# Kernel optimization log

Hardware: AMD Instinct MI355X
Metric: run time of the kernel (lower is better)

## Reference

```python
import jax, jax.numpy as jnp
import numpy as np
import math

NQ = 8            # n_qubits (hardcoded in _TransformerBlockQuantum)
DIM = 2 ** NQ     # statevector size = 256
H = 16            # num_heads
EPS = 1e-5        # LayerNorm eps

# PauliZ expectation table: wire 0 = most significant bit. ZTAB[w, j] = +/-1
_bits = (np.arange(DIM)[None, :] >> (NQ - 1 - np.arange(NQ)[:, None])) & 1
ZTAB = (1.0 - 2.0 * _bits).astype(np.float32)  # [NQ, DIM]


def _apply_1q(state, gate, w):
    # state: [N, 2^NQ] complex, gate: [N, 2, 2] complex, acts on wire w (MSB ordering)
    N = state.shape[0]
    s = state.reshape(N, 2 ** w, 2, 2 ** (NQ - w - 1))
    s = jnp.einsum('nab,npbq->npaq', gate, s)
    return s.reshape(N, DIM)


def _apply_cnot(state, c):
    # CNOT with control wire c, target wire c+1 (adjacent chain)
    N = state.shape[0]
    s = state.reshape(N, 2 ** c, 2, 2, 2 ** (NQ - c - 2))
    s = jnp.concatenate([s[:, :, :1], jnp.flip(s[:, :, 1:], axis=3)], axis=2)
    return s.reshape(N, DIM)


def _layernorm(x, g, b):
    mu = jnp.mean(x, axis=-1, keepdims=True)
    var = jnp.mean((x - mu) ** 2, axis=-1, keepdims=True)
    return (x - mu) / jnp.sqrt(var + EPS) * g + b


def _quantum_ffn(x, Win, b_in, Wout, b_out, ry):
    B, S, D = x.shape
    ang = (jnp.einsum('bsd,qd->bsq', x, Win) + b_in).reshape(-1, NQ)  # [N, NQ]
    N = ang.shape[0]
    state = jnp.zeros((N, DIM), jnp.complex64).at[:, 0].set(1.0)
    # RX encoding (per-token angles)
    for w in range(NQ):
        th = ang[:, w] * 0.5
        c, s = jnp.cos(th), jnp.sin(th)
        g = jnp.stack([jnp.stack([c, -1j * s], -1), jnp.stack([-1j * s, c], -1)], -2)
        state = _apply_1q(state, g.astype(jnp.complex64), w)
    # trainable RY (shared angles)
    for w in range(NQ):
        th = ry[w] * 0.5
        c, s = jnp.cos(th), jnp.sin(th)
        g = jnp.stack([jnp.stack([c, -s]), jnp.stack([s, c])]).astype(jnp.complex64)
        state = _apply_1q(state, jnp.broadcast_to(g, (N, 2, 2)), w)
    # CNOT entangling chain
    for w in range(NQ - 1):
        state = _apply_cnot(state, w)
    probs = jnp.abs(state) ** 2                      # [N, DIM] float32
    expz = probs @ ZTAB.T                            # [N, NQ]
    out = jnp.einsum('bsq,dq->bsd', expz.reshape(B, S, NQ), Wout) + b_out
    return jax.nn.relu(out)  # dropout = identity in eval


def _forward(x, Wq, Wk, Wv, Wo, g1, b1, g2, b2, Win, b_in, Wout, b_out, ry):
    B, S, D = x.shape
    dk = D // H
    q = jnp.einsum('bsd,ed->bse', x, Wq).reshape(B, S, H, dk)
    k = jnp.einsum('bsd,ed->bse', x, Wk).reshape(B, S, H, dk)
    v = jnp.einsum('bsd,ed->bse', x, Wv).reshape(B, S, H, dk)
    scores = jnp.einsum('bqhd,bkhd->bhqk', q, k) / math.sqrt(dk)
    attn = jax.nn.softmax(scores, axis=-1)
    o = jnp.einsum('bhqk,bkhd->bqhd', attn, v).reshape(B, S, D)
    attn_out = jnp.einsum('bsd,ed->bse', o, Wo)
    x1 = _layernorm(x + attn_out, g1, b1)
    ffn_out = _quantum_ffn(x1, Win, b_in, Wout, b_out, ry)
    return _layernorm(x1 + ffn_out, g2, b2)


def setup_inputs() -> dict:
    key = jax.random.key(0)
    ks = jax.random.split(key, 16)
    B, S, D = 2, 2048, 1024
    sd = 1.0 / math.sqrt(D)
    return {
        'x': jax.random.normal(ks[0], (B, S, D), jnp.float32),
        'Wq': jax.random.normal(ks[1], (D, D), jnp.float32) * sd,
        'Wk': jax.random.normal(ks[2], (D, D), jnp.float32) * sd,
        'Wv': jax.random.normal(ks[3], (D, D), jnp.float32) * sd,
        'Wo': jax.random.normal(ks[4], (D, D), jnp.float32) * sd,
        'g1': jnp.ones((D,), jnp.float32),
        'b1': jnp.zeros((D,), jnp.float32),
        'g2': jnp.ones((D,), jnp.float32),
        'b2': jnp.zeros((D,), jnp.float32),
        'Win': jax.random.normal(ks[5], (NQ, D), jnp.float32) * sd,
        'b_in': jnp.zeros((NQ,), jnp.float32),
        'Wout': jax.random.normal(ks[6], (D, NQ), jnp.float32) * (1.0 / math.sqrt(NQ)),
        'b_out': jnp.zeros((D,), jnp.float32),
        'ry': jax.random.normal(ks[7], (NQ,), jnp.float32) * 0.1,
    }


def reference(x, Wq, Wk, Wv, Wo, g1, b1, g2, b2, Win, b_in, Wout, b_out, ry):
    return _forward(x, Wq, Wk, Wv, Wo, g1, b1, g2, b2, Win, b_in, Wout, b_out, ry)
```

## Files before the change

kernel.cpp:

```cpp
#include <hip/hip_runtime.h>
#include <stdint.h>


typedef unsigned short u16;
typedef unsigned int   u32;
typedef __bf16 bf16x8 __attribute__((ext_vector_type(8)));
typedef u16    u16x8  __attribute__((ext_vector_type(8)));
typedef u16    u16x4  __attribute__((ext_vector_type(4)));
typedef float  f32x4  __attribute__((ext_vector_type(4)));

#define DEV static __device__ __forceinline__

DEV u16 f2b(float f){ u32 u = __float_as_uint(f); return (u16)((u + 0x7fffu + ((u>>16)&1u)) >> 16); }

#define MFMA16(a,b,c) __builtin_amdgcn_mfma_f32_16x16x32_bf16((a),(b),(c),0,0,0)
#define GLD16(gp,lp) __builtin_amdgcn_global_load_lds( \
    (const __attribute__((address_space(1))) u32*)(const void*)(gp), \
    (__attribute__((address_space(3))) u32*)(void*)(lp), 16, 0, 0)

__global__ __launch_bounds__(256) void k_cast(const float* __restrict__ src, u16* __restrict__ dst){
  const int i = blockIdx.x*256 + threadIdx.x;
  const f32x4* s = (const f32x4*)src + (size_t)i*2;
  f32x4 a = s[0], b = s[1];
  u16x8 o;
  o[0]=f2b(a.x); o[1]=f2b(a.y); o[2]=f2b(a.z); o[3]=f2b(a.w);
  o[4]=f2b(b.x); o[5]=f2b(b.y); o[6]=f2b(b.z); o[7]=f2b(b.w);
  ((u16x8*)dst)[i] = o;
}

__global__ __launch_bounds__(256) void k_cast_w(
    const float* __restrict__ Wq, const float* __restrict__ Wk,
    const float* __restrict__ Wv, const float* __restrict__ Wo,
    u16* __restrict__ wb, u16* __restrict__ wob){
  const int r = blockIdx.x >> 9, bi = blockIdx.x & 511;
  const float* src = (r==0)?Wq:((r==1)?Wk:((r==2)?Wv:Wo));
  u16* dst = (r<3) ? (wb + (size_t)r*1048576) : wob;
  const int i = bi*256 + threadIdx.x;
  const f32x4* s = (const f32x4*)src + (size_t)i*2;
  f32x4 a = s[0], b = s[1];
  u16x8 o;
  o[0]=f2b(a.x); o[1]=f2b(a.y); o[2]=f2b(a.z); o[3]=f2b(a.w);
  o[4]=f2b(b.x); o[5]=f2b(b.y); o[6]=f2b(b.z); o[7]=f2b(b.w);
  ((u16x8*)dst)[i] = o;
}

template<int MODE>
__global__ __launch_bounds__(256) void k_gemm_nt(
    const u16* __restrict__ A, const u16* __restrict__ B,
    float* __restrict__ Cf, u16* __restrict__ Qo, u16* __restrict__ Ko, u16* __restrict__ Vt,
    int K, int N)
{
  __shared__ __attribute__((aligned(16))) u16 As[128*64];
  __shared__ __attribute__((aligned(16))) u16 Bs[128*64];
  const int tid = threadIdx.x, lane = tid & 63, w = tid >> 6;
  const int wr = w >> 1, wc = w & 1;
  const int m0 = blockIdx.y*128, n0 = blockIdx.x*128;
  const int l15 = lane & 15, lg = lane >> 4;
  f32x4 acc[4][4] = {};
  const int lr = lane >> 3, lc = (lane & 7)*8;
  const u16* ag = A + (size_t)(m0 + w*32 + lr)*K + lc;
  const u16* bg = B + (size_t)(n0 + w*32 + lr)*K + lc;
  u16* asl = &As[(w*32)*64];
  u16* bsl = &Bs[(w*32)*64];
  for (int k0 = 0; k0 < K; k0 += 64){
    __syncthreads();
    #pragma unroll
    for (int c = 0; c < 4; ++c){
      GLD16(ag + (size_t)(c*8)*K + k0, asl + c*512);
      GLD16(bg + (size_t)(c*8)*K + k0, bsl + c*512);
    }
    __syncthreads();
    #pragma unroll
    for (int kk = 0; kk < 2; ++kk){
      const int ko = kk*32 + lg*8;
      bf16x8 af[4], bf[4];
      #pragma unroll
      for (int t=0;t<4;++t) af[t] = *(const bf16x8*)&As[(wr*64 + t*16 + l15)*64 + ko];
      #pragma unroll
      for (int t=0;t<4;++t) bf[t] = *(const bf16x8*)&Bs[(wc*64 + t*16 + l15)*64 + ko];
      #pragma unroll
      for (int i=0;i<4;++i)
        #pragma unroll
        for (int j=0;j<4;++j)
          acc[i][j] = MFMA16(af[i], bf[j], acc[i][j]);
    }
  }
  const int col0 = n0 + wc*64 + l15;
  const int row0 = m0 + wr*64 + lg*4;
  if (MODE==0){
    const int which = n0 >> 10;
    if (which == 2){
      #pragma unroll
      for (int i=0;i<4;++i){
        const int rr0 = row0 + i*16;
        const int bsel = rr0 >> 11, ss = rr0 & 2047;
        #pragma unroll
        for (int j=0;j<4;++j){
          const int d_loc = (col0 + j*16) & 1023;
          const int hh = d_loc >> 6, dd = d_loc & 63;
          u16x4 pk;
          #pragma unroll
          for (int r=0;r<4;++r) pk[r] = f2b(acc[i][j][r]);
          *(u16x4*)(Vt + ((size_t)((bsel*16 + hh)*64 + dd))*2048 + ss) = pk;
        }
      }
    } else {
      u16* dst = which ? Ko : Qo;
      const float scl = which ? 1.f : 0.125f;
      #pragma unroll
      for (int i=0;i<4;++i)
      #pragma unroll
      for (int j=0;j<4;++j){
        const int cc = (col0 + j*16) & 1023;
        #pragma unroll
        for (int r=0;r<4;++r)
          dst[(size_t)(row0 + i*16 + r)*1024 + cc] = f2b(acc[i][j][r]*scl);
      }
    }
  } else {
    #pragma unroll
    for (int i=0;i<4;++i)
    #pragma unroll
    for (int j=0;j<4;++j){
      const int cc = col0 + j*16;
      #pragma unroll
      for (int r=0;r<4;++r)
        Cf[(size_t)(row0 + i*16 + r)*N + cc] = acc[i][j][r];
    }
  }
}

__global__ __launch_bounds__(256) void k_attn(
    const u16* __restrict__ q, const u16* __restrict__ k,
    const u16* __restrict__ vt, u16* __restrict__ o)
{
  __shared__ __attribute__((aligned(16))) char KVb[2][16384];
  __shared__ __attribute__((aligned(16))) u16 Ps[4][1024];
  const int tid = threadIdx.x, lane = tid & 63, w = tid >> 6;
  const int p = blockIdx.x >> 5, qt = blockIdx.x & 31;
  const int b = p >> 4, h = p & 15;
  const int t0 = b*2048 + qt*64 + w*16;
  const int l15 = lane & 15, lg = lane >> 4;
  const int swz = (l15 & 7) << 4;
  bf16x8 qa[2];
  #pragma unroll
  for (int kk=0;kk<2;++kk)
    qa[kk] = *(const bf16x8*)(q + (size_t)(t0 + l15)*1024 + h*64 + kk*32 + lg*8);
  const char* kgl[2]; const char* vgl[2]; int ldsK[2], ldsV[2];
  #pragma unroll
  for (int i=0;i<2;++i){
    const int s = w*2048 + i*1024 + lane*16;
    const int row = s >> 7;
    const int cb = (s & 127) ^ ((row & 7) << 4);
    kgl[i] = (const char*)k  + ((size_t)(b*2048 + row))*2048 + h*128 + cb;
    vgl[i] = (const char*)vt + ((size_t)(p*64    + row))*4096 + cb;
    ldsK[i] = w*2048 + i*1024;
    ldsV[i] = 8192 + w*2048 + i*1024;
  }
  f32x4 oacc[4] = {};
  float mrow = -1e30f, lrow = 0.f;
  int cur = 0;
  #pragma unroll
  for (int i=0;i<2;++i){ GLD16(kgl[i], KVb[0] + ldsK[i]); GLD16(vgl[i], KVb[0] + ldsV[i]); }
  for (int it = 0; it < 32; ++it){
    __syncthreads();
    if (it < 31){
      const size_t nkv = (size_t)(it+1)*64;
      #pragma unroll
      for (int i=0;i<2;++i){
        GLD16(kgl[i] + nkv*2048, KVb[cur^1] + ldsK[i]);
        GLD16(vgl[i] + nkv*2,    KVb[cur^1] + ldsV[i]);
      }
    }
    const char* Kb = KVb[cur];
    const char* Vb = KVb[cur] + 8192;
    f32x4 sacc[4] = {};
    #pragma unroll
    for (int kk=0;kk<2;++kk){
      const int co = (kk*64 + lg*16) ^ swz;
      bf16x8 kbf[4];
      #pragma unroll
      for (int nt=0;nt<4;++nt) kbf[nt] = *(const bf16x8*)(Kb + (nt*16 + l15)*128 + co);
      #pragma unroll
      for (int nt=0;nt<4;++nt) sacc[nt] = MFMA16(kbf[nt], qa[kk], sacc[nt]);
    }
    float mx = sacc[0][0];
    #pragma unroll
    for (int nt=0;nt<4;++nt)
      #pragma unroll
      for (int r=0;r<4;++r) mx = fmaxf(mx, sacc[nt][r]);
    mx = fmaxf(mx, __shfl_xor(mx, 16));
    mx = fmaxf(mx, __shfl_xor(mx, 32));
    const float mnew = fmaxf(mrow, mx);
    const float scl = __expf(mrow - mnew);
    mrow = mnew;
    float rsum = 0.f;
    #pragma unroll
    for (int nt=0;nt<4;++nt)
      #pragma unroll
      for (int r=0;r<4;++r){ float e = __expf(sacc[nt][r] - mnew); sacc[nt][r] = e; rsum += e; }
    rsum += __shfl_xor(rsum, 16);
    rsum += __shfl_xor(rsum, 32);
    lrow = lrow*scl + rsum;
    char* Pw = (char*)&Ps[w][0];
    #pragma unroll
    for (int nt=0;nt<4;++nt){
      u16x4 pk;
      #pragma unroll
      for (int r=0;r<4;++r) pk[r] = f2b(sacc[nt][r]);
      *(u16x4*)(Pw + l15*128 + (((nt*16 + lg*4)*2) ^ swz)) = pk;
    }
    float sclo[4];
    #pragma unroll
    for (int r=0;r<4;++r) sclo[r] = __shfl(scl, lg*4 + r);
    #pragma unroll
    for (int nt=0;nt<4;++nt)
      #pragma unroll
      for (int r=0;r<4;++r) oacc[nt][r] *= sclo[r];
    #pragma unroll
    for (int kk=0;kk<2;++kk){
      const int co = (kk*64 + lg*16) ^ swz;
      bf16x8 pf = *(const bf16x8*)(Pw + l15*128 + co);
      bf16x8 vf[4];
      #pragma unroll
      for (int nt=0;nt<4;++nt) vf[nt] = *(const bf16x8*)(Vb + (nt*16 + l15)*128 + co);
      #pragma unroll
      for (int nt=0;nt<4;++nt) oacc[nt] = MFMA16(pf, vf[nt], oacc[nt]);
    }
    cur ^= 1;
  }
  float rl[4];
  #pragma unroll
  for (int r=0;r<4;++r){ float lf = __shfl(lrow, lg*4 + r); rl[r] = 1.f/lf; }
  #pragma unroll
  for (int nt=0;nt<4;++nt)
  #pragma unroll
  for (int r=0;r<4;++r)
    o[(size_t)(t0 + lg*4 + r)*1024 + h*64 + nt*16 + l15] = f2b(oacc[nt][r]*rl[r]);
}

__global__ __launch_bounds__(256) void k_tail(
    const float* __restrict__ x, const float* __restrict__ attn,
    const float* __restrict__ g1, const float* __restrict__ b1,
    const float* __restrict__ Win, const float* __restrict__ b_in,
    const float* __restrict__ Wout, const float* __restrict__ b_out,
    const float* __restrict__ ry,
    const float* __restrict__ g2, const float* __restrict__ b2,
    float* __restrict__ out)
{
  const int tid = threadIdx.x, lane = tid & 63, w = tid >> 6;
  const int t = blockIdx.x*4 + w;
  const size_t base = (size_t)t*1024;
  f32x4 yv[4];
  float s1 = 0.f, s2 = 0.f;
  #pragma unroll
  for (int c=0;c<4;++c){
    const int idx = c*256 + lane*4;
    f32x4 xv = *(const f32x4*)(x + base + idx);
    f32x4 av = *(const f32x4*)(attn + base + idx);
    f32x4 y = xv + av;
    yv[c] = y;
    s1 += y.x + y.y + y.z + y.w;
    s2 += y.x*y.x + y.y*y.y + y.z*y.z + y.w*y.w;
  }
  #pragma unroll
  for (int off=32; off; off>>=1){ s1 += __shfl_xor(s1, off); s2 += __shfl_xor(s2, off); }
  {
    const float mu = s1*(1.f/1024.f);
    const float rinv = rsqrtf(s2*(1.f/1024.f) - mu*mu + 1e-5f);
    #pragma unroll
    for (int c=0;c<4;++c){
      const int idx = c*256 + lane*4;
      f32x4 gv = *(const f32x4*)(g1 + idx);
      f32x4 bv = *(const f32x4*)(b1 + idx);
      f32x4 y = yv[c];
      y.x = (y.x-mu)*rinv*gv.x + bv.x;
      y.y = (y.y-mu)*rinv*gv.y + bv.y;
      y.z = (y.z-mu)*rinv*gv.z + bv.z;
      y.w = (y.w-mu)*rinv*gv.w + bv.w;
      yv[c] = y;
    }
  }
  float ang[8];
  #pragma unroll
  for (int qq=0; qq<8; ++qq){
    float acc = 0.f;
    #pragma unroll
    for (int c=0;c<4;++c){
      f32x4 wv = *(const f32x4*)(Win + qq*1024 + c*256 + lane*4);
      acc += wv.x*yv[c].x + wv.y*yv[c].y + wv.z*yv[c].z + wv.w*yv[c].w;
    }
    ang[qq] = acc;
  }
  #pragma unroll
  for (int off=32; off; off>>=1)
    #pragma unroll
    for (int qq=0; qq<8; ++qq) ang[qq] += __shfl_xor(ang[qq], off);
  #pragma unroll
  for (int qq=0; qq<8; ++qq) ang[qq] += b_in[qq];
  float vr[4], vi[4];
  #pragma unroll
  for (int r=0;r<4;++r){ vr[r]=0.f; vi[r]=0.f; }
  if (lane==0) vr[0] = 1.f;
  #pragma unroll
  for (int wi=0; wi<8; ++wi){
    float s, c; __sincosf(ang[wi]*0.5f, &s, &c);
    const int pbit = 7 - wi;
    if (pbit >= 6){
      const int rp = 1 << (pbit-6);
      #pragma unroll
      for (int r=0;r<4;++r) if (!(r & rp)){
        const int r2 = r | rp;
        float ar=vr[r], ai=vi[r], br=vr[r2], bi=vi[r2];
        vr[r]  = c*ar + s*bi;  vi[r]  = c*ai - s*br;
        vr[r2] = c*br + s*ai;  vi[r2] = c*bi - s*ar;
      }
    } else {
      const int msk = 1 << pbit;
      #pragma unroll
      for (int r=0;r<4;++r){
        float orr = __shfl_xor(vr[r], msk);
        float oii = __shfl_xor(vi[r], msk);
        float nr = c*vr[r] + s*oii;
        float ni = c*vi[r] - s*orr;
        vr[r]=nr; vi[r]=ni;
      }
    }
  }
  #pragma unroll
  for (int wi=0; wi<8; ++wi){
    float s, c; __sincosf(ry[wi]*0.5f, &s, &c);
    const int pbit = 7 - wi;
    if (pbit >= 6){
      const int rp = 1 << (pbit-6);
      #pragma unroll
      for (int r=0;r<4;++r) if (!(r & rp)){
        const int r2 = r | rp;
        float ar=vr[r], ai=vi[r], br=vr[r2], bi=vi[r2];
        vr[r]  = c*ar - s*br;  vi[r]  = c*ai - s*bi;
        vr[r2] = s*ar + c*br;  vi[r2] = s*ai + c*bi;
      }
    } else {
      const int msk = 1 << pbit;
      const float sg = (lane & msk) ? s : -s;
      #pragma unroll
      for (int r=0;r<4;++r){
        float orr = __shfl_xor(vr[r], msk);
        float oii = __shfl_xor(vi[r], msk);
        float nr = c*vr[r] + sg*orr;
        float ni = c*vi[r] + sg*oii;
        vr[r]=nr; vi[r]=ni;
      }
    }
  }
  { float tr=vr[2]; vr[2]=vr[3]; vr[3]=tr; float ti=vi[2]; vi[2]=vi[3]; vi[3]=ti; }
  vr[1]=__shfl_xor(vr[1],32); vi[1]=__shfl_xor(vi[1],32);
  vr[3]=__shfl_xor(vr[3],32); vi[3]=__shfl_xor(vi[3],32);
  #pragma unroll
  for (int cn=2; cn<7; ++cn){
    const int pc = 7-cn, pt = pc-1;
    const bool ctl = (lane >> pc) & 1;
    #pragma unroll
    for (int r=0;r<4;++r){
      float tr = __shfl_xor(vr[r], 1<<pt);
      float ti = __shfl_xor(vi[r], 1<<pt);
      if (ctl){ vr[r]=tr; vi[r]=ti; }
    }
  }
  float pr[4];
  #pragma unroll
  for (int r=0;r<4;++r) pr[r] = vr[r]*vr[r] + vi[r]*vi[r];
  float e[8];
  e[0] = (pr[0]+pr[1]) - (pr[2]+pr[3]);
  e[1] = (pr[0]+pr[2]) - (pr[1]+pr[3]);
  const float tot = pr[0]+pr[1]+pr[2]+pr[3];
  #pragma unroll
  for (int wi=2; wi<8; ++wi){
    const int pbit = 7-wi;
    e[wi] = ((lane >> pbit) & 1) ? -tot : tot;
  }
  #pragma unroll
  for (int off=1; off<64; off<<=1)
    #pragma unroll
    for (int i=0;i<8;++i) e[i] += __shfl_xor(e[i], off);
  float yy[4][4];
  s1 = 0.f; s2 = 0.f;
  #pragma unroll
  for (int c=0;c<4;++c){
    const float x1a[4] = {yv[c].x, yv[c].y, yv[c].z, yv[c].w};
    #pragma unroll
    for (int j=0;j<4;++j){
      const int d = c*256 + lane*4 + j;
      f32x4 w0 = *(const f32x4*)(Wout + (size_t)d*8);
      f32x4 w1 = *(const f32x4*)(Wout + (size_t)d*8 + 4);
      float acc = b_out[d];
      acc += w0.x*e[0] + w0.y*e[1] + w0.z*e[2] + w0.w*e[3];
      acc += w1.x*e[4] + w1.y*e[5] + w1.z*e[6] + w1.w*e[7];
      const float y = x1a[j] + fmaxf(acc, 0.f);
      yy[c][j] = y;
      s1 += y; s2 += y*y;
    }
  }
  #pragma unroll
  for (int off=32; off; off>>=1){ s1 += __shfl_xor(s1, off); s2 += __shfl_xor(s2, off); }
  const float mu = s1*(1.f/1024.f);
  const float rinv = rsqrtf(s2*(1.f/1024.f) - mu*mu + 1e-5f);
  #pragma unroll
  for (int c=0;c<4;++c){
    const int idx = c*256 + lane*4;
    f32x4 gv = *(const f32x4*)(g2 + idx);
    f32x4 bv = *(const f32x4*)(b2 + idx);
    f32x4 ov;
    ov.x = (yy[c][0]-mu)*rinv*gv.x + bv.x;
    ov.y = (yy[c][1]-mu)*rinv*gv.y + bv.y;
    ov.z = (yy[c][2]-mu)*rinv*gv.z + bv.z;
    ov.w = (yy[c][3]-mu)*rinv*gv.w + bv.w;
    *(f32x4*)(out + base + idx) = ov;
  }
}

extern "C" void kernel_launch(void* const* d_in, const int* in_sizes, int n_in,
                              void* d_out, int out_size, void* d_ws, size_t ws_size,
                              hipStream_t stream)
{
  const float* x    = (const float*)d_in[0];
  const float* Wq   = (const float*)d_in[1];
  const float* Wk   = (const float*)d_in[2];
  const float* Wv   = (const float*)d_in[3];
  const float* Wo   = (const float*)d_in[4];
  const float* g1   = (const float*)d_in[5];
  const float* b1   = (const float*)d_in[6];
  const float* g2   = (const float*)d_in[7];
  const float* b2   = (const float*)d_in[8];
  const float* Win  = (const float*)d_in[9];
  const float* b_in = (const float*)d_in[10];
  const float* Wout = (const float*)d_in[11];
  const float* b_out= (const float*)d_in[12];
  const float* ry   = (const float*)d_in[13];
  float* out = (float*)d_out;
  char* ws = (char*)d_ws;
  const size_t MB = 1024u*1024u;
  u16* xb  = (u16*)(ws + 0*MB);
  u16* wb  = (u16*)(ws + 8*MB);
  u16* wob = (u16*)(ws + 14*MB);
  u16* qb  = (u16*)(ws + 16*MB);
  u16* kb  = (u16*)(ws + 24*MB);
  u16* vtb = (u16*)(ws + 32*MB);
  u16* ob  = (u16*)(ws + 40*MB);
  float* attn_out = (float*)(ws + 48*MB);

  k_cast<<<2048, 256, 0, stream>>>(x, xb);
  k_cast_w<<<2048, 256, 0, stream>>>(Wq, Wk, Wv, Wo, wb, wob);
  k_gemm_nt<0><<<dim3(24,32), 256, 0, stream>>>(xb, wb, nullptr, qb, kb, vtb, 1024, 3072);
  k_attn<<<1024, 256, 0, stream>>>(qb, kb, vtb, ob);
  k_gemm_nt<1><<<dim3(8,32), 256, 0, stream>>>(ob, wob, attn_out, nullptr, nullptr, nullptr, 1024, 1024);
  k_tail<<<1024, 256, 0, stream>>>(x, attn_out, g1, b1, Win, b_in, Wout, b_out, ry, g2, b2, out);
}
```

Before: 279.2 us.

## Double attention query rows per wave, use exp2 softmax with lazy rescale

Result: faster. 270.4 us (-3.1%).

```diff
diff --git a/kernel.cpp b/kernel.cpp
--- a/kernel.cpp
+++ b/kernel.cpp
@@ -12,6 +12,8 @@
 #define DEV static __device__ __forceinline__
 
 DEV u16 f2b(float f){ u32 u = __float_as_uint(f); return (u16)((u + 0x7fffu + ((u>>16)&1u)) >> 16); }
+DEV u16 b2u(__bf16 h){ union{__bf16 b; u16 u;} c; c.b = h; return c.u; }
+DEV float exp2fast(float x){ return __builtin_amdgcn_exp2f(x); }
 
 #define MFMA16(a,b,c) __builtin_amdgcn_mfma_f32_16x16x32_bf16((a),(b),(c),0,0,0)
 #define GLD16(gp,lp) __builtin_amdgcn_global_load_lds( \
@@ -106,7 +108,7 @@
       }
     } else {
       u16* dst = which ? Ko : Qo;
-      const float scl = which ? 1.f : 0.125f;
+      const float scl = which ? 1.f : 0.125f*1.44269504f;
       #pragma unroll
       for (int i=0;i<4;++i)
       #pragma unroll
@@ -135,17 +137,19 @@
     const u16* __restrict__ vt, u16* __restrict__ o)
 {
   __shared__ __attribute__((aligned(16))) char KVb[2][16384];
-  __shared__ __attribute__((aligned(16))) u16 Ps[4][1024];
+  __shared__ __attribute__((aligned(16))) u16 Ps[4][2048];
   const int tid = threadIdx.x, lane = tid & 63, w = tid >> 6;
-  const int p = blockIdx.x >> 5, qt = blockIdx.x & 31;
+  const int p = blockIdx.x >> 4, qt = blockIdx.x & 15;
   const int b = p >> 4, h = p & 15;
-  const int t0 = b*2048 + qt*64 + w*16;
+  const int t0 = b*2048 + qt*128 + w*32;
   const int l15 = lane & 15, lg = lane >> 4;
   const int swz = (l15 & 7) << 4;
-  bf16x8 qa[2];
+  bf16x8 qa[2][2];
+  #pragma unroll
+  for (int mt=0;mt<2;++mt)
   #pragma unroll
   for (int kk=0;kk<2;++kk)
-    qa[kk] = *(const bf16x8*)(q + (size_t)(t0 + l15)*1024 + h*64 + kk*32 + lg*8);
+    qa[mt][kk] = *(const bf16x8*)(q + (size_t)(t0 + mt*16 + l15)*1024 + h*64 + kk*32 + lg*8);
   const char* kgl[2]; const char* vgl[2]; int ldsK[2], ldsV[2];
   #pragma unroll
   for (int i=0;i<2;++i){
@@ -157,8 +161,8 @@
     ldsK[i] = w*2048 + i*1024;
     ldsV[i] = 8192 + w*2048 + i*1024;
   }
-  f32x4 oacc[4] = {};
-  float mrow = -1e30f, lrow = 0.f;
+  f32x4 oacc[2][4] = {};
+  float mrow[2] = {-1e30f, -1e30f}, lrow[2] = {0.f, 0.f};
   int cur = 0;
   #pragma unroll
   for (int i=0;i<2;++i){ GLD16(kgl[i], KVb[0] + ldsK[i]); GLD16(vgl[i], KVb[0] + ldsV[i]); }
@@ -174,7 +178,7 @@
     }
     const char* Kb = KVb[cur];
     const char* Vb = KVb[cur] + 8192;
-    f32x4 sacc[4] = {};
+    f32x4 sacc[2][4] = {};
     #pragma unroll
     for (int kk=0;kk<2;++kk){
       const int co = (kk*64 + lg*16) ^ swz;
@@ -182,61 +186,90 @@
       #pragma unroll
       for (int nt=0;nt<4;++nt) kbf[nt] = *(const bf16x8*)(Kb + (nt*16 + l15)*128 + co);
       #pragma unroll
-      for (int nt=0;nt<4;++nt) sacc[nt] = MFMA16(kbf[nt], qa[kk], sacc[nt]);
-    }
-    float mx = sacc[0][0];
-    #pragma unroll
-    for (int nt=0;nt<4;++nt)
-      #pragma unroll
-      for (int r=0;r<4;++r) mx = fmaxf(mx, sacc[nt][r]);
-    mx = fmaxf(mx, __shfl_xor(mx, 16));
-    mx = fmaxf(mx, __shfl_xor(mx, 32));
-    const float mnew = fmaxf(mrow, mx);
-    const float scl = __expf(mrow - mnew);
-    mrow = mnew;
-    float rsum = 0.f;
-    #pragma unroll
-    for (int nt=0;nt<4;++nt)
-      #pragma unroll
-      for (int r=0;r<4;++r){ float e = __expf(sacc[nt][r] - mnew); sacc[nt][r] = e; rsum += e; }
-    rsum += __shfl_xor(rsum, 16);
-    rsum += __shfl_xor(rsum, 32);
-    lrow = lrow*scl + rsum;
+      for (int mt=0;mt<2;++mt)
+      #pragma unroll
+      for (int nt=0;nt<4;++nt)
+        sacc[mt][nt] = MFMA16(kbf[nt], qa[mt][kk], sacc[mt][nt]);
+    }
+    float mx[2];
+    #pragma unroll
+    for (int mt=0;mt<2;++mt){
+      float m = sacc[mt][0][0];
+      #pragma unroll
+      for (int nt=0;nt<4;++nt)
+        #pragma unroll
+        for (int r=0;r<4;++r) m = fmaxf(m, sacc[mt][nt][r]);
+      m = fmaxf(m, __shfl_xor(m, 16));
+      m = fmaxf(m, __shfl_xor(m, 32));
+      mx[mt] = m;
+    }
+    const int ok = (mx[0] <= mrow[0] + 8.f) && (mx[1] <= mrow[1] + 8.f);
+    if (!__all(ok)){
+      #pragma unroll
+      for (int mt=0;mt<2;++mt){
+        const float mnew = fmaxf(mrow[mt], mx[mt]);
+        const float scl = exp2fast(mrow[mt] - mnew);
+        mrow[mt] = mnew;
+        lrow[mt] *= scl;
+        float sclo[4];
+        #pragma unroll
+        for (int r=0;r<4;++r) sclo[r] = __shfl(scl, lg*4 + r);
+        #pragma unroll
+        for (int nt=0;nt<4;++nt)
+          #pragma unroll
+          for (int r=0;r<4;++r) oacc[mt][nt][r] *= sclo[r];
+      }
+    }
     char* Pw = (char*)&Ps[w][0];
     #pragma unroll
-    for (int nt=0;nt<4;++nt){
-      u16x4 pk;
-      #pragma unroll
-      for (int r=0;r<4;++r) pk[r] = f2b(sacc[nt][r]);
-      *(u16x4*)(Pw + l15*128 + (((nt*16 + lg*4)*2) ^ swz)) = pk;
-    }
-    float sclo[4];
-    #pragma unroll
-    for (int r=0;r<4;++r) sclo[r] = __shfl(scl, lg*4 + r);
-    #pragma unroll
-    for (int nt=0;nt<4;++nt)
-      #pragma unroll
-      for (int r=0;r<4;++r) oacc[nt][r] *= sclo[r];
+    for (int mt=0;mt<2;++mt){
+      float rsum = 0.f;
+      #pragma unroll
+      for (int nt=0;nt<4;++nt)
+        #pragma unroll
+        for (int r=0;r<4;++r){
+          float e = exp2fast(sacc[mt][nt][r] - mrow[mt]);
+          sacc[mt][nt][r] = e;
+          rsum += e;
+        }
+      rsum += __shfl_xor(rsum, 16);
+      rsum += __shfl_xor(rsum, 32);
+      lrow[mt] += rsum;
+      #pragma unroll
+      for (int nt=0;nt<4;++nt){
+        u16x4 pk;
+        #pragma unroll
+        for (int r=0;r<4;++r) pk[r] = b2u((__bf16)sacc[mt][nt][r]);
+        *(u16x4*)(Pw + (mt*16 + l15)*128 + (((nt*16 + lg*4)*2) ^ swz)) = pk;
+      }
+    }
     #pragma unroll
     for (int kk=0;kk<2;++kk){
       const int co = (kk*64 + lg*16) ^ swz;
-      bf16x8 pf = *(const bf16x8*)(Pw + l15*128 + co);
-      bf16x8 vf[4];
+      bf16x8 pf[2], vf[4];
+      #pragma unroll
+      for (int mt=0;mt<2;++mt) pf[mt] = *(const bf16x8*)(Pw + (mt*16 + l15)*128 + co);
       #pragma unroll
       for (int nt=0;nt<4;++nt) vf[nt] = *(const bf16x8*)(Vb + (nt*16 + l15)*128 + co);
       #pragma unroll
-      for (int nt=0;nt<4;++nt) oacc[nt] = MFMA16(pf, vf[nt], oacc[nt]);
+      for (int mt=0;mt<2;++mt)
+      #pragma unroll
+      for (int nt=0;nt<4;++nt)
+        oacc[mt][nt] = MFMA16(pf[mt], vf[nt], oacc[mt][nt]);
     }
     cur ^= 1;
   }
-  float rl[4];
-  #pragma unroll
-  for (int r=0;r<4;++r){ float lf = __shfl(lrow, lg*4 + r); rl[r] = 1.f/lf; }
-  #pragma unroll
-  for (int nt=0;nt<4;++nt)
-  #pragma unroll
-  for (int r=0;r<4;++r)
-    o[(size_t)(t0 + lg*4 + r)*1024 + h*64 + nt*16 + l15] = f2b(oacc[nt][r]*rl[r]);
+  #pragma unroll
+  for (int mt=0;mt<2;++mt){
+    float rl[4];
+    #pragma unroll
+    for (int r=0;r<4;++r){ float lf = __shfl(lrow[mt], lg*4 + r); rl[r] = 1.f/lf; }
+    #pragma unroll
+    for (int nt=0;nt<4;++nt)
+    #pragma unroll
+    for (int r=0;r<4;++r)
+      o[(size_t)(t0 + mt*16 + lg*4 + r)*1024 + h*64 + nt*16 + l15] = b2u((__bf16)(oacc[mt][nt][r]*rl[r]));
+  }
 }
 
 __global__ __launch_bounds__(256) void k_tail(
@@ -452,7 +485,7 @@
   k_cast<<<2048, 256, 0, stream>>>(x, xb);
   k_cast_w<<<2048, 256, 0, stream>>>(Wq, Wk, Wv, Wo, wb, wob);
   k_gemm_nt<0><<<dim3(24,32), 256, 0, stream>>>(xb, wb, nullptr, qb, kb, vtb, 1024, 3072);
-  k_attn<<<1024, 256, 0, stream>>>(qb, kb, vtb, ob);
+  k_attn<<<512, 256, 0, stream>>>(qb, kb, vtb, ob);
   k_gemm_nt<1><<<dim3(8,32), 256, 0, stream>>>(ob, wob, attn_out, nullptr, nullptr, nullptr, 1024, 1024);
   k_tail<<<1024, 256, 0, stream>>>(x, attn_out, g1, b1, Win, b_in, Wout, b_out, ry, g2, b2, out);
 }
```
